# Optimization experiments

Measured on AMD Instinct MI355X. Metric: run time of the kernel, lower is better.

The kernel has to match this reference:

```python
import jax, jax.numpy as jnp
import numpy as np

B = 8          # batch
HID = 1024     # hidden_size
NH = 8         # query heads
KVH = 1        # kv heads (GQA)
HD = 256       # head_dim
NL = 18        # layers
MLP = 4096     # intermediate size
AH = 50        # action_horizon (suffix len)
AD = 32        # action_dim
P = 1037       # prefix_len
EPS = 1e-6
ROPE_BASE = 10000.0
SCALE = HD ** -0.5
NEG = -2.3819763e38


def _rms(x):
    return x * jax.lax.rsqrt(jnp.mean(x * x, axis=-1, keepdims=True) + EPS)


def _ada_norm(x, cond, W):
    # AdaRMS: cond -> (scale, shift, gate); normed*(1+scale)+shift, gate returned for gated residual
    scale, shift, gate = jnp.split(cond @ W, 3, axis=-1)
    return _rms(x) * (1.0 + scale[:, None, :]) + shift[:, None, :], gate[:, None, :]


def _rope(x, pos):
    # x: [B, heads, S, HD], pos: [B, S]; HF rotate-half convention
    inv = 1.0 / (ROPE_BASE ** (jnp.arange(0, HD, 2, dtype=jnp.float32) / HD))
    freqs = pos[:, :, None].astype(jnp.float32) * inv          # [B,S,HD/2]
    cos = jnp.tile(jnp.cos(freqs), (1, 1, 2))[:, None]          # [B,1,S,HD]
    sin = jnp.tile(jnp.sin(freqs), (1, 1, 2))[:, None]
    x1, x2 = jnp.split(x, 2, axis=-1)
    return x * cos + jnp.concatenate([-x2, x1], axis=-1) * sin


def setup_inputs() -> dict:
    key = jax.random.key(0)
    ks = jax.random.split(key, 24)
    s = 0.02
    return {
        'prefix_keys': jax.random.normal(ks[0], (B, NL, KVH, P, HD), jnp.float32),
        'prefix_values': jax.random.normal(ks[1], (B, NL, KVH, P, HD), jnp.float32),
        'prefix_pad_masks': jnp.ones((B, P), dtype=bool),
        'x_t': jax.random.normal(ks[2], (B, AH, AD), jnp.float32),
        'timestep': jax.random.uniform(ks[3], (B,), jnp.float32),
        'Wq': jax.random.normal(ks[4], (NL, HID, NH * HD), jnp.float32) * s,
        'Wk': jax.random.normal(ks[5], (NL, HID, KVH * HD), jnp.float32) * s,
        'Wv': jax.random.normal(ks[6], (NL, HID, KVH * HD), jnp.float32) * s,
        'Wo': jax.random.normal(ks[7], (NL, NH * HD, HID), jnp.float32) * s,
        'Wg': jax.random.normal(ks[8], (NL, HID, MLP), jnp.float32) * s,
        'Wu': jax.random.normal(ks[9], (NL, HID, MLP), jnp.float32) * s,
        'Wd': jax.random.normal(ks[10], (NL, MLP, HID), jnp.float32) * s,
        'A1': jax.random.normal(ks[11], (NL, HID, 3 * HID), jnp.float32) * s,
        'A2': jax.random.normal(ks[12], (NL, HID, 3 * HID), jnp.float32) * s,
        'Af': jax.random.normal(ks[13], (HID, 3 * HID), jnp.float32) * s,
        'W_act_in': jax.random.normal(ks[14], (AD, HID), jnp.float32) * s,
        'b_act_in': jnp.zeros((HID,), jnp.float32),
        'W_act_out': jax.random.normal(ks[15], (HID, AD), jnp.float32) * s,
        'b_act_out': jnp.zeros((AD,), jnp.float32),
        'W_t_in': jax.random.normal(ks[16], (HID, HID), jnp.float32) * s,
        'b_t_in': jnp.zeros((HID,), jnp.float32),
        'W_t_out': jax.random.normal(ks[17], (HID, HID), jnp.float32) * s,
        'b_t_out': jnp.zeros((HID,), jnp.float32),
    }


def reference(prefix_keys, prefix_values, prefix_pad_masks, x_t, timestep,
              Wq, Wk, Wv, Wo, Wg, Wu, Wd, A1, A2, Af,
              W_act_in, b_act_in, W_act_out, b_act_out,
              W_t_in, b_t_in, W_t_out, b_t_out):
    b = x_t.shape[0]
    # --- time embedding (sinusoidal over log-spaced periods) -> AdaRMS cond ---
    frac = jnp.linspace(0.0, 1.0, HID // 2)
    period = 0.004 * (4.0 / 0.004) ** frac
    sin_in = (2.0 * jnp.pi / period)[None, :] * timestep[:, None]
    temb = jnp.concatenate([jnp.sin(sin_in), jnp.cos(sin_in)], axis=1)  # [B,HID]
    cond = jax.nn.silu(jax.nn.silu(temb @ W_t_in + b_t_in) @ W_t_out + b_t_out)

    # --- action input projection ---
    h = x_t @ W_act_in + b_act_in  # [B,AH,HID]

    # --- attention mask & positions ---
    # suffix att_masks = [1,0,...,0] -> cumsum constant -> suffix block fully visible
    suf_att = jnp.ones((b, AH, AH), dtype=bool)
    s2p = jnp.broadcast_to(prefix_pad_masks[:, None, :], (b, AH, P))
    full = jnp.concatenate([s2p, suf_att], axis=2)          # [B,AH,P+AH]
    bias = jnp.where(full, 0.0, NEG).astype(jnp.float32)[:, None]  # [B,1,AH,P+AH]
    offs = jnp.sum(prefix_pad_masks.astype(jnp.int32), axis=-1, keepdims=True)
    pos = offs + jnp.arange(AH)                              # [B,AH]

    def layer(hcur, p):
        wq, wk, wv, wo, wg, wu, wd, a1, a2, ck, cv = p
        normed, gate = _ada_norm(hcur, cond, a1)
        q = (normed @ wq).reshape(b, AH, NH, HD).transpose(0, 2, 1, 3)
        k = (normed @ wk).reshape(b, AH, KVH, HD).transpose(0, 2, 1, 3)
        v = (normed @ wv).reshape(b, AH, KVH, HD).transpose(0, 2, 1, 3)
        q = _rope(q, pos)
        k = _rope(k, pos)
        fk = jnp.concatenate([ck, k], axis=2)   # [B,KVH,P+AH,HD]
        fv = jnp.concatenate([cv, v], axis=2)
        rep = NH // KVH
        fk = jnp.repeat(fk, rep, axis=1)
        fv = jnp.repeat(fv, rep, axis=1)
        scores = jnp.einsum('bhqd,bhkd->bhqk', q, fk) * SCALE + bias
        attn = jax.nn.softmax(scores, axis=-1)
        o = jnp.einsum('bhqk,bhkd->bhqd', attn, fv)
        o = o.transpose(0, 2, 1, 3).reshape(b, AH, NH * HD) @ wo
        h1 = hcur + gate * o                     # gated residual 1
        n2, gate2 = _ada_norm(h1, cond, a2)
        mlp = (jax.nn.gelu(n2 @ wg, approximate=True) * (n2 @ wu)) @ wd
        return h1 + gate2 * mlp, None            # gated residual 2

    pk = jnp.moveaxis(prefix_keys, 1, 0)   # [NL,B,KVH,P,HD]
    pv = jnp.moveaxis(prefix_values, 1, 0)
    h, _ = jax.lax.scan(layer, h, (Wq, Wk, Wv, Wo, Wg, Wu, Wd, A1, A2, pk, pv))

    out, _ = _ada_norm(h, cond, Af)
    return out @ W_act_out + b_act_out  # [B,AH,AD]
```

## Files before the change

### kernel.cpp

```cpp
#include <hip/hip_runtime.h>

typedef unsigned short u16;
typedef unsigned int   u32;
typedef __attribute__((ext_vector_type(8))) short bh8;
typedef __attribute__((ext_vector_type(4))) float f4;

constexpr int BATCH = 8, HIDN = 1024, NHEAD = 8, HD = 256, NLAY = 18, DMLP = 4096;
constexpr int AHOR = 50, ADIMN = 32, PFXN = 1037, SEQN = 1087, NSTR = 17, MR = 400, MP = 512;
constexpr float EPSV = 1e-6f, NEGV = -2.3819763e38f, QSCALE = 0.0625f;
constexpr size_t ADASL = (size_t)37 * 3 * BATCH * HIDN;
constexpr int SW64 = 90, SW32 = 138, SKT = 266, SPT = 74, SVT = 90;

static __device__ __forceinline__ u16 f2bf(float x){
  union{float f; u32 u;} v; v.f = x;
  u32 r = (v.u + 0x7FFFu + ((v.u >> 16) & 1u)) >> 16;
  return (u16)r;
}
static __device__ __forceinline__ float bf2f(u16 u){
  union{u32 u; float f;} v; v.u = ((u32)u) << 16; return v.f;
}
static __device__ __forceinline__ u32 pack2(float a, float b){
  return (u32)f2bf(a) | ((u32)f2bf(b) << 16);
}
static __device__ __forceinline__ f4 MFMA(bh8 a, bh8 b, f4 c){
  return __builtin_amdgcn_mfma_f32_16x16x32_bf16(a, b, c, 0, 0, 0);
}
static __device__ __forceinline__ float siluf_(float x){ return x / (1.f + __expf(-x)); }
static __device__ __forceinline__ float geluf_(float x){
  float y = 0.7978845608028654f * (x + 0.044715f * x * x * x);
  float e = __expf(2.f * y);
  return 0.5f * x * (2.f - 2.f / (e + 1.f));
}

__global__ void k_prep(const int* __restrict__ mask, const float* __restrict__ ts,
                       float* __restrict__ temb, int* __restrict__ offs,
                       float* __restrict__ ropec, float* __restrict__ ropes)
{
  int t = threadIdx.x;
  {
    int b = t >> 5, l = t & 31;
    const int* mp = mask + b * PFXN;
    int s = 0;
    for (int k = l; k < PFXN; k += 32) s += (mp[k] != 0);
    #pragma unroll
    for (int off = 16; off >= 1; off >>= 1) s += __shfl_xor(s, off);
    if (l == 0) offs[b] = s;
  }
  for (int i = t; i < BATCH * 512; i += 256){
    int b = i >> 9, j = i & 511;
    float frac = (float)j * (1.0f / 511.0f);
    float period = 0.004f * __expf(frac * 6.907755278982137f);
    float arg = (6.283185307179586f / period) * ts[b];
    float s, c; sincosf(arg, &s, &c);
    temb[b * HIDN + j] = s;
    temb[b * HIDN + 512 + j] = c;
  }
  __syncthreads();
  for (int i = t; i < BATCH * AHOR * 128; i += 256){
    int d = i & 127, bt = i >> 7, b = bt / AHOR, tt = bt % AHOR;
    float inv = __expf(-((float)d * (1.f / 128.f)) * 9.210340371976184f);
    float arg = (float)(offs[b] + tt) * inv;
// ... 97 lines not shown
  float* hp = h + (size_t)r * HIDN + c0;
  hp[0] = a0; hp[1] = a1; hp[2] = a2; hp[3] = a3;
}

__global__ void k_resnorm(int mode, int np,
    const float* __restrict__ base, const u16* __restrict__ parts,
    const float* __restrict__ gate, const float* __restrict__ sc,
    const float* __restrict__ sh, float* __restrict__ outres,
    u16* __restrict__ fragA)
{
  __shared__ float redl[4];
  int t = threadIdx.x;
  int c = t * 4;
  for (int i = 0; i < 2; ++i){
    int r = blockIdx.x * 2 + i;
    bool live = (r < MR);
    float4 v = {0.f,0.f,0.f,0.f};
    int b = live ? (r / AHOR) : 0;
    if (live){
      v = *(const float4*)(base + (size_t)r * HIDN + c);
      if (mode){
        float s0 = 0, s1 = 0, s2 = 0, s3 = 0;
        #pragma unroll 4
        for (int p = 0; p < np; ++p){
          ushort4 u4 = *(const ushort4*)(parts + ((size_t)p * MP + r) * HIDN + c);
          s0 += bf2f(u4.x); s1 += bf2f(u4.y); s2 += bf2f(u4.z); s3 += bf2f(u4.w);
        }
        float4 gp = *(const float4*)(gate + b * HIDN + c);
        v.x += gp.x * s0; v.y += gp.y * s1; v.z += gp.z * s2; v.w += gp.w * s3;
        *(float4*)(outres + (size_t)r * HIDN + c) = v;
      }
    }
    float ss = v.x*v.x + v.y*v.y + v.z*v.z + v.w*v.w;
    #pragma unroll
    for (int off = 1; off < 64; off <<= 1) ss += __shfl_xor(ss, off);
    if ((t & 63) == 0) redl[t >> 6] = ss;
    __syncthreads();
    float tot = redl[0] + redl[1] + redl[2] + redl[3];
    __syncthreads();
    u16* dst = fragA + ((size_t)(c >> 3)) * MP * 8 + (size_t)r * 8 + (c & 7);
    ushort4 ov;
    if (live){
      float rstd = rsqrtf(tot * (1.0f / HIDN) + EPSV);
      const float4 scp = *(const float4*)(sc + b * HIDN + c);
      const float4 shp = *(const float4*)(sh + b * HIDN + c);
      ov.x = f2bf(v.x * rstd * (1.f + scp.x) + shp.x);
      ov.y = f2bf(v.y * rstd * (1.f + scp.y) + shp.y);
      ov.z = f2bf(v.z * rstd * (1.f + scp.z) + shp.z);
      ov.w = f2bf(v.w * rstd * (1.f + scp.w) + shp.w);
    } else {
      ov.x = ov.y = ov.z = ov.w = 0;
    }
    *(ushort4*)dst = ov;
  }
}

template<int NOUTER>
static __device__ __forceinline__ void gemm_core64(
    const u16* __restrict__ fa,
    const float* __restrict__ Wa, int cb0,
    const float* __restrict__ Wb, int cb1,
    int wN, int kc0, u16* lds, f4 acc[4][4])
{
  const int tid = threadIdx.x;
  const int lane = tid & 63, wave = tid >> 6;
  const int l15 = lane & 15, g = lane >> 4;
  const int wrow = wave * 64;
  const int c4 = (tid & 15) * 4;
  const int r0 = (tid >> 4) * 2;
  const float* wcol = (c4 < 32) ? (Wa + cb0 + c4) : (Wb + cb1 + (c4 - 32));
  const size_t krow0 = (size_t)kc0 * 8 + r0;
  f4 preA[3], preB[3];
  bh8 ab[2][2][4];
  preA[0] = *(const f4*)(wcol + krow0 * wN);
  preB[0] = *(const f4*)(wcol + (krow0 + 1) * wN);
  #pragma unroll
  for (int kk = 0; kk < 2; ++kk){
    const u16* ap = fa + ((size_t)(kc0 + kk * 4 + g) * MP + wrow + l15) * 8;
    #pragma unroll
    for (int mf = 0; mf < 4; ++mf) ab[0][kk][mf] = *(const bh8*)(ap + mf * 128);
  }
  if (NOUTER > 1){
    preA[1] = *(const f4*)(wcol + (krow0 + 64) * wN);
    preB[1] = *(const f4*)(wcol + (krow0 + 65) * wN);
  }
  if (NOUTER > 2){
    preA[2] = *(const f4*)(wcol + (krow0 + 128) * wN);
    preB[2] = *(const f4*)(wcol + (krow0 + 129) * wN);
  }
  #pragma unroll
  for (int i = 0; i < 4; ++i)
    *(u32*)(lds + (c4 + i) * SW64 + r0) = pack2(preA[0][i], preB[0][i]);
  __syncthreads();
  #pragma unroll
  for (int ko = 0; ko < NOUTER; ++ko){
    u16* ldsr = lds + (ko & 1) * (64 * SW64);
    if (ko + 1 < NOUTER){
      #pragma unroll
      for (int kk = 0; kk < 2; ++kk){
        const u16* ap = fa + ((size_t)(kc0 + (ko + 1) * 8 + kk * 4 + g) * MP + wrow + l15) * 8;
        #pragma unroll
        for (int mf = 0; mf < 4; ++mf) ab[(ko + 1) & 1][kk][mf] = *(const bh8*)(ap + mf * 128);
      }
    }
    if (ko + 3 < NOUTER){
      preA[ko % 3] = *(const f4*)(wcol + (krow0 + (size_t)(ko + 3) * 64) * wN);
      preB[ko % 3] = *(const f4*)(wcol + (krow0 + (size_t)(ko + 3) * 64 + 1) * wN);
    }
    #pragma unroll
    for (int kk = 0; kk < 2; ++kk){
      bh8 bb[4];
      #pragma unroll
      for (int nf = 0; nf < 4; ++nf) bb[nf] = *(const bh8*)(ldsr + (nf * 16 + l15) * SW64 + kk * 32 + g * 8);
      #pragma unroll
      for (int mf = 0; mf < 4; ++mf)
        #pragma unroll
        for (int nf = 0; nf < 4; ++nf)
          acc[mf][nf] = MFMA(ab[ko & 1][kk][mf], bb[nf], acc[mf][nf]);
    }
    if (ko + 1 < NOUTER){
      u16* ldsw = lds + ((ko + 1) & 1) * (64 * SW64);
      const int sl = (ko + 1) % 3;
      #pragma unroll
      for (int i = 0; i < 4; ++i)
        *(u32*)(ldsw + (c4 + i) * SW64 + r0) = pack2(preA[sl][i], preB[sl][i]);
      __syncthreads();
    }
  }
}

template<int NOUTER>
static __device__ __forceinline__ void gemm_core32w(
    const u16* __restrict__ fa,
    const float* __restrict__ Wa, int cb0,
    const float* __restrict__ Wb, int cb1,
    int wN, u16* lds, f4 acc[4][2])
{
  const int tid = threadIdx.x;
  const int lane = tid & 63, wave = tid >> 6;
  const int l15 = lane & 15, g = lane >> 4;
  const int wrow = wave * 64;
  const int c4 = (tid & 7) * 4;
  const int r0 = (tid >> 3) * 2;
  const float* wcol = (c4 < 16) ? (Wa + cb0 + c4) : (Wb + cb1 + (c4 - 16));
  f4 preA[3], preB[3];
  preA[0] = *(const f4*)(wcol + (size_t)r0 * wN);
  preB[0] = *(const f4*)(wcol + (size_t)(r0 + 1) * wN);
  if (NOUTER > 1){
    preA[1] = *(const f4*)(wcol + (size_t)(128 + r0) * wN);
    preB[1] = *(const f4*)(wcol + (size_t)(129 + r0) * wN);
  }
  if (NOUTER > 2){
    preA[2] = *(const f4*)(wcol + (size_t)(256 + r0) * wN);
    preB[2] = *(const f4*)(wcol + (size_t)(257 + r0) * wN);
  }
  #pragma unroll
  for (int i = 0; i < 4; ++i)
    *(u32*)(lds + (c4 + i) * SW32 + r0) = pack2(preA[0][i], preB[0][i]);
  __syncthreads();
  #pragma unroll
  for (int ko = 0; ko < NOUTER; ++ko){
    u16* ldsr = lds + (ko & 1) * (32 * SW32);
    bh8 a01[2][4], a23[2][4];
    #pragma unroll
    for (int kk = 0; kk < 2; ++kk){
      const u16* ap = fa + ((size_t)(ko * 16 + kk * 4 + g) * MP + wrow + l15) * 8;
      #pragma unroll
      for (int mf = 0; mf < 4; ++mf) a01[kk][mf] = *(const bh8*)(ap + mf * 128);
    }
    if (ko + 3 < NOUTER){
      preA[ko % 3] = *(const f4*)(wcol + (size_t)((ko + 3) * 128 + r0) * wN);
      preB[ko % 3] = *(const f4*)(wcol + (size_t)((ko + 3) * 128 + r0 + 1) * wN);
    }
    #pragma unroll
    for (int kk = 2; kk < 4; ++kk){
      const u16* ap = fa + ((size_t)(ko * 16 + kk * 4 + g) * MP + wrow + l15) * 8;
      #pragma unroll
      for (int mf = 0; mf < 4; ++mf) a23[kk - 2][mf] = *(const bh8*)(ap + mf * 128);
    }
    #pragma unroll
// ... 44 lines not shown
  f4 acc[4][2];
  #pragma unroll
  for (int i = 0; i < 4; ++i)
    #pragma unroll
    for (int j = 0; j < 2; ++j) acc[i][j] = (f4){0.f, 0.f, 0.f, 0.f};
  gemm_core32w<8>(n1, Wa, cb0, Wb, cb1, wN, lds, acc);
  int tid = threadIdx.x, lane = tid & 63, wave = tid >> 6, l15 = lane & 15, g = lane >> 4;
  int wrow = wave * 64;
  #pragma unroll
  for (int mf = 0; mf < 4; ++mf)
    #pragma unroll
    for (int r = 0; r < 4; ++r){
      int row = wrow + mf * 16 + 4 * g + r;
      if (row >= MR) continue;
      int b = row / AHOR, tt = row - b * AHOR;
      float lo = acc[mf][0][r], hi = acc[mf][1][r];
      if (type == 2){
        size_t vb = ((size_t)(b * AHOR + tt)) * HD;
        vs[vb + d0 + l15] = f2bf(lo);
        vs[vb + d0 + 16 + l15] = f2bf(hi);
      } else {
        int dA = fb + l15;
        float cz = ropec[(size_t)(b * AHOR + tt) * 128 + dA];
        float sz = ropes[(size_t)(b * AHOR + tt) * 128 + dA];
        float oA = lo * cz - hi * sz;
        float oB = hi * cz + lo * sz;
        if (type == 0){
          oA *= QSCALE; oB *= QSCALE;
          int rowp = head * AHOR + tt;
          int dB = dA + 128;
          qf[((size_t)(b * 32 + (dA >> 3))) * MP * 8 + (size_t)rowp * 8 + (dA & 7)] = f2bf(oA);
          qf[((size_t)(b * 32 + (dB >> 3))) * MP * 8 + (size_t)rowp * 8 + (dB & 7)] = f2bf(oB);
        } else {
          size_t kb = ((size_t)(b * AHOR + tt)) * HD;
          ks[kb + dA] = f2bf(oA);
          ks[kb + dA + 128] = f2bf(oB);
        }
      }
    }
}

__global__ __launch_bounds__(512) void k_attn(
    const u16* __restrict__ qf, const u16* __restrict__ kss, const u16* __restrict__ vss,
    const float* __restrict__ pk, const float* __restrict__ pv,
    const int* __restrict__ mask, int layer,
    u16* __restrict__ opart, float* __restrict__ mrow, float* __restrict__ lrow)
{
  __shared__ u16 kv[256 * SVT];
  __shared__ u16 plds[256 * SPT];
  int s = blockIdx.x, b = blockIdx.y, z = blockIdx.z;
  int tid = threadIdx.x, lane = tid & 63, wave = tid >> 6, l15 = lane & 15, g = lane >> 4;
  int zb = z * 256;
  int wbase = wave * 32;
  {
    int key = tid >> 3, dblk = (tid & 7) * 32;
    int kg = s * 64 + key;
    u32* dst = (u32*)(kv + key * SKT + dblk);
    if (kg < PFXN){
      const float4* src = (const float4*)(pk + (((size_t)b * NLAY + layer) * PFXN + kg) * HD + dblk);
      #pragma unroll
      for (int j = 0; j < 8; ++j){ float4 v = src[j]; dst[2*j] = pack2(v.x, v.y); dst[2*j+1] = pack2(v.z, v.w); }
    } else if (kg < SEQN){
      const u32* src = (const u32*)(kss + ((size_t)b * AHOR + (kg - PFXN)) * HD + dblk);
      #pragma unroll
      for (int j = 0; j < 16; ++j) dst[j] = src[j];
    } else {
      #pragma unroll
      for (int j = 0; j < 16; ++j) dst[j] = 0;
    }
  }
  float vreg[32];
  int vkey = tid >> 3, vdb = (tid & 7) * 32;
  {
    int kgv = s * 64 + vkey;
    if (kgv < PFXN){
      const float4* src = (const float4*)(pv + (((size_t)b * NLAY + layer) * PFXN + kgv) * HD + vdb);
      #pragma unroll
      for (int j = 0; j < 8; ++j){ float4 v = src[j]; vreg[4*j] = v.x; vreg[4*j+1] = v.y; vreg[4*j+2] = v.z; vreg[4*j+3] = v.w; }
    } else if (kgv < SEQN){
      const u32* src = (const u32*)(vss + ((size_t)b * AHOR + (kgv - PFXN)) * HD + vdb);
      #pragma unroll
      for (int j = 0; j < 16; ++j){ u32 u = src[j]; vreg[2*j] = bf2f((u16)(u & 0xFFFF)); vreg[2*j+1] = bf2f((u16)(u >> 16)); }
    } else {
      #pragma unroll
      for (int j = 0; j < 32; ++j) vreg[j] = 0.f;
    }
  }
  bool valid[4];
  #pragma unroll
  for (int nf = 0; nf < 4; ++nf){
    int kgc = s * 64 + nf * 16 + l15;
    valid[nf] = (kgc < PFXN) ? (mask[b * PFXN + kgc] != 0) : (kgc < SEQN);
  }
  __syncthreads();
  f4 acc[2][4];
  #pragma unroll
  for (int i = 0; i < 2; ++i)
    #pragma unroll
    for (int j = 0; j < 4; ++j) acc[i][j] = (f4){0.f,0.f,0.f,0.f};
  const u16* qb = qf + (size_t)b * 32 * MP * 8;
  #pragma unroll
  for (int ko = 0; ko < 4; ++ko)
    #pragma unroll
    for (int kk = 0; kk < 2; ++kk){
      int kc = ko * 8 + kk * 4 + g;
      bh8 a[2], bb[4];
      const u16* ap = qb + ((size_t)kc * MP + zb + wbase + l15) * 8;
      #pragma unroll
      for (int mf = 0; mf < 2; ++mf) a[mf] = *(const bh8*)(ap + mf * 128);
      #pragma unroll
      for (int nf = 0; nf < 4; ++nf) bb[nf] = *(const bh8*)(kv + (nf * 16 + l15) * SKT + ko * 64 + kk * 32 + g * 8);
      #pragma unroll
      for (int mf = 0; mf < 2; ++mf)
        #pragma unroll
        for (int nf = 0; nf < 4; ++nf) acc[mf][nf] = MFMA(a[mf], bb[nf], acc[mf][nf]);
    }
  #pragma unroll
  for (int nf = 0; nf < 4; ++nf) if (!valid[nf]){
    #pragma unroll
    for (int mf = 0; mf < 2; ++mf){
      acc[mf][nf][0] = NEGV; acc[mf][nf][1] = NEGV; acc[mf][nf][2] = NEGV; acc[mf][nf][3] = NEGV;
    }
  }
  #pragma unroll
  for (int mf = 0; mf < 2; ++mf)
    #pragma unroll
    for (int r = 0; r < 4; ++r){
      float m0 = fmaxf(fmaxf(acc[mf][0][r], acc[mf][1][r]), fmaxf(acc[mf][2][r], acc[mf][3][r]));
      #pragma unroll
      for (int off = 1; off < 16; off <<= 1) m0 = fmaxf(m0, __shfl_xor(m0, off));
      int lr = wbase + mf * 16 + 4 * g + r;
      float sum = 0.f;
      #pragma unroll
      for (int nf = 0; nf < 4; ++nf){
        float p = __expf(acc[mf][nf][r] - m0);
        sum += p;
        plds[lr * SPT + nf * 16 + l15] = f2bf(p);
      }
      #pragma unroll
      for (int off = 1; off < 16; off <<= 1) sum += __shfl_xor(sum, off);
      if (l15 == 0){
        mrow[((size_t)b * NSTR + s) * MP + zb + lr] = m0;
        lrow[((size_t)b * NSTR + s) * MP + zb + lr] = sum;
      }
    }
  __syncthreads();
  {
    #pragma unroll
    for (int j = 0; j < 32; ++j){
      int dloc = vdb + j;
      kv[dloc * SVT + ((dloc >> 5) & 3) * 8 + vkey] = f2bf(vreg[j]);
    }
  }
  __syncthreads();
  #pragma unroll
  for (int dc = 0; dc < 4; ++dc){
    f4 oc[2][4];
    #pragma unroll
    for (int i = 0; i < 2; ++i)
      #pragma unroll
      for (int j = 0; j < 4; ++j) oc[i][j] = (f4){0.f,0.f,0.f,0.f};
    #pragma unroll
    for (int kk = 0; kk < 2; ++kk){
      bh8 a[2], bb[4];
      #pragma unroll
      for (int mf = 0; mf < 2; ++mf) a[mf] = *(const bh8*)(plds + (wbase + mf * 16 + l15) * SPT + kk * 32 + g * 8);
      #pragma unroll
      for (int nf = 0; nf < 4; ++nf){
        int dcol = dc * 64 + nf * 16 + l15;
        bb[nf] = *(const bh8*)(kv + dcol * SVT + ((dcol >> 5) & 3) * 8 + kk * 32 + g * 8);
      }
      #pragma unroll
      for (int mf = 0; mf < 2; ++mf)
        #pragma unroll
        for (int nf = 0; nf < 4; ++nf) oc[mf][nf] = MFMA(a[mf], bb[nf], oc[mf][nf]);
    }
    #pragma unroll
    for (int mf = 0; mf < 2; ++mf)
      #pragma unroll
      for (int r = 0; r < 4; ++r){
        int row = zb + wbase + mf * 16 + 4 * g + r;
        if (row < MR){
          #pragma unroll
          for (int nf = 0; nf < 4; ++nf){
            int d = dc * 64 + nf * 16 + l15;
            opart[(((size_t)b * NSTR + s) * MR + row) * HD + d] = f2bf(oc[mf][nf][r]);
          }
        }
      }
  }
}

__global__ void k_comb(const u16* __restrict__ opart, const float* __restrict__ mrow,
                       const float* __restrict__ lrow, u16* __restrict__ ao)
{
  int b = blockIdx.y;
  int t = threadIdx.x;
  int d4 = (t & 63) * 4;
  int row = blockIdx.x * 4 + (t >> 6);
  float M = -3.0e38f;
  for (int s2 = 0; s2 < NSTR; ++s2) M = fmaxf(M, mrow[((size_t)b * NSTR + s2) * MP + row]);
  float L = 0.f;
  float o0 = 0.f, o1 = 0.f, o2 = 0.f, o3 = 0.f;
  for (int s2 = 0; s2 < NSTR; ++s2){
    float w = __expf(mrow[((size_t)b * NSTR + s2) * MP + row] - M);
    L += w * lrow[((size_t)b * NSTR + s2) * MP + row];
    ushort4 u4 = *(const ushort4*)(opart + (((size_t)b * NSTR + s2) * MR + row) * HD + d4);
    o0 += w * bf2f(u4.x); o1 += w * bf2f(u4.y); o2 += w * bf2f(u4.z); o3 += w * bf2f(u4.w);
  }
  float rL = 1.0f / L;
  int h = row / AHOR, tt = row - h * AHOR;
  int col = h * HD + d4;
  int rg = b * AHOR + tt;
  ushort4 ov;
  ov.x = f2bf(o0 * rL); ov.y = f2bf(o1 * rL); ov.z = f2bf(o2 * rL); ov.w = f2bf(o3 * rL);
  *(ushort4*)(ao + ((size_t)(col >> 3)) * MP * 8 + (size_t)rg * 8 + (col & 7)) = ov;
}

template<int NOUTER>
__global__ __launch_bounds__(512) void k_gemm_part(
    const u16* __restrict__ fa, const float* __restrict__ W, int wN,
    int kcPerSlice, u16* __restrict__ outp)
{
  __shared__ u16 lds[2 * 64 * SW64];
  int n0 = blockIdx.x * 64;
  int ksl = blockIdx.y;
  f4 acc[4][4];
  #pragma unroll
  for (int i = 0; i < 4; ++i)
    #pragma unroll
    for (int j = 0; j < 4; ++j) acc[i][j] = (f4){0.f,0.f,0.f,0.f};
  gemm_core64<NOUTER>(fa, W, n0, W, n0 + 32, wN, ksl * kcPerSlice, lds, acc);
  int tid = threadIdx.x, lane = tid & 63, wave = tid >> 6, l15 = lane & 15, g = lane >> 4;
  int wrow = wave * 64;
  #pragma unroll
  for (int mf = 0; mf < 4; ++mf)
    #pragma unroll
    for (int r = 0; r < 4; ++r){
      int row = wrow + mf * 16 + 4 * g + r;
      #pragma unroll
      for (int nf = 0; nf < 4; ++nf)
        outp[((size_t)ksl * MP + row) * 1024 + n0 + nf * 16 + l15] = f2bf(acc[mf][nf][r]);
    }
}

__global__ __launch_bounds__(512) void k_mlpup(
    const u16* __restrict__ n2, const float* __restrict__ Wg, const float* __restrict__ Wu,
    u16* __restrict__ mlpf)
{
  __shared__ u16 lds[2 * 32 * SW32];
  int n0 = blockIdx.x * 16;
  f4 acc[4][2];
  #pragma unroll
  for (int i = 0; i < 4; ++i)
    #pragma unroll
    for (int j = 0; j < 2; ++j) acc[i][j] = (f4){0.f,0.f,0.f,0.f};
  gemm_core32w<8>(n2, Wg, n0, Wu, n0, DMLP, lds, acc);
  int tid = threadIdx.x, lane = tid & 63, wave = tid >> 6, l15 = lane & 15, g = lane >> 4;
  int wrow = wave * 64;
  #pragma unroll
  for (int mf = 0; mf < 4; ++mf)
    #pragma unroll
    for (int r = 0; r < 4; ++r){
      int row = wrow + mf * 16 + 4 * g + r;
      int col = n0 + l15;
      float gg = acc[mf][0][r], uu = acc[mf][1][r];
      float act = geluf_(gg) * uu;
      mlpf[((size_t)(col >> 3)) * MP * 8 + (size_t)row * 8 + (col & 7)] = f2bf(act);
    }
}

__global__ void k_out(const u16* __restrict__ nfr, const float* __restrict__ W,
                      const float* __restrict__ bias, float* __restrict__ out)
{
  int t = threadIdx.x;
  int row = blockIdx.x * 8 + (t >> 5);
  int c = t & 31;
  float acc = bias[c];
  for (int kc = 0; kc < 128; ++kc){
    bh8 v = *(const bh8*)(nfr + ((size_t)kc * MP + row) * 8);
    #pragma unroll
    for (int j = 0; j < 8; ++j)
      acc += bf2f((u16)v[j]) * W[(kc * 8 + j) * ADIMN + c];
  }
  out[row * ADIMN + c] = acc;
}

extern "C" void kernel_launch(void* const* d_in, const int* in_sizes, int n_in,
                              void* d_out, int out_size, void* d_ws, size_t ws_size,
                              hipStream_t stream)
{
  const float* pk  = (const float*)d_in[0];
  const float* pv  = (const float*)d_in[1];
  const int*   msk = (const int*)d_in[2];
  const float* xt  = (const float*)d_in[3];
  const float* ts  = (const float*)d_in[4];
  const float* Wq  = (const float*)d_in[5];
  const float* Wk  = (const float*)d_in[6];
  const float* Wv  = (const float*)d_in[7];
  const float* Wo  = (const float*)d_in[8];
  const float* Wg  = (const float*)d_in[9];
  const float* Wu  = (const float*)d_in[10];
  const float* Wd  = (const float*)d_in[11];
  const float* A1  = (const float*)d_in[12];
  const float* A2  = (const float*)d_in[13];
  const float* Af  = (const float*)d_in[14];
  const float* Wai = (const float*)d_in[15];
  const float* bai = (const float*)d_in[16];
  const float* Wao = (const float*)d_in[17];
  const float* bao = (const float*)d_in[18];
  const float* Wti = (const float*)d_in[19];
  const float* bti = (const float*)d_in[20];
  const float* Wto = (const float*)d_in[21];
  const float* bto = (const float*)d_in[22];

  char* w = (char*)d_ws;
  size_t off = 0;
  auto alloc = [&](size_t bytes) -> char* {
    char* p = w + off; off += (bytes + 255) & ~(size_t)255; return p;
  };
  float* temb  = (float*)alloc((size_t)BATCH * HIDN * 4);
  float* ttmp  = (float*)alloc((size_t)BATCH * HIDN * 4);
  float* cond  = (float*)alloc((size_t)BATCH * HIDN * 4);
  int*   offs  = (int*)alloc(BATCH * 4);
  float* ropec = (float*)alloc((size_t)BATCH * AHOR * 128 * 4);
  float* ropes = (float*)alloc((size_t)BATCH * AHOR * 128 * 4);
  float* ada   = (float*)alloc(ADASL * 4);
  float* adap  = (float*)alloc(8 * ADASL * 4);
  float* h     = (float*)alloc((size_t)MR * HIDN * 4);
  float* h1    = (float*)alloc((size_t)MR * HIDN * 4);
  u16*   n1    = (u16*)alloc((size_t)128 * MP * 8 * 2);
  u16*   n2    = (u16*)alloc((size_t)128 * MP * 8 * 2);
  u16*   qf    = (u16*)alloc((size_t)BATCH * 32 * MP * 8 * 2);
  u16*   kss   = (u16*)alloc((size_t)BATCH * AHOR * HD * 2);
  u16*   vss   = (u16*)alloc((size_t)BATCH * AHOR * HD * 2);
  u16*   opart = (u16*)alloc((size_t)BATCH * NSTR * MR * HD * 2);
  float* mrow  = (float*)alloc((size_t)BATCH * NSTR * MP * 4);
  float* lrow  = (float*)alloc((size_t)BATCH * NSTR * MP * 4);
  u16*   ao    = (u16*)alloc((size_t)256 * MP * 8 * 2);
  u16*   opp   = (u16*)alloc((size_t)16 * MP * 1024 * 2);
  u16*   mlpf  = (u16*)alloc((size_t)512 * MP * 8 * 2);
  u16*   mdp   = (u16*)alloc((size_t)16 * MP * 1024 * 2);
  if (off > ws_size) return;

  k_prep<<<1, 256, 0, stream>>>(msk, ts, temb, offs, ropec, ropes);
  k_tproj<<<32, 256, 0, stream>>>(temb, Wti, bti, ttmp);
  k_tproj<<<32, 256, 0, stream>>>(ttmp, Wto, bto, cond);
  k_ada_part<<<dim3(3, 37, 8), 256, 0, stream>>>(cond, A1, A2, Af, adap);
  k_ada_red<<<444, 256, 0, stream>>>(adap, ada);
  k_hin<<<MR, 256, 0, stream>>>(xt, Wai, bai, h);

  auto AP = [&](int y, int comp){ return ada + ((size_t)y * 3 + comp) * BATCH * HIDN; };

  k_resnorm<<<256, 256, 0, stream>>>(0, 0, h, nullptr, nullptr, AP(0,0), AP(0,1), nullptr, n1);

  for (int l = 0; l < NLAY; ++l){
    k_qkvrope<<<80, 512, 0, stream>>>(n1, Wq + (size_t)l * HIDN * NHEAD * HD,
                                      Wk + (size_t)l * HIDN * HD, Wv + (size_t)l * HIDN * HD,
                                      ropec, ropes, qf, kss, vss);
    k_attn<<<dim3(NSTR, BATCH, 2), 512, 0, stream>>>(qf, kss, vss, pk, pv, msk, l, opart, mrow, lrow);
    k_comb<<<dim3(100, BATCH), 256, 0, stream>>>(opart, mrow, lrow, ao);
    k_gemm_part<2><<<dim3(16, 16), 512, 0, stream>>>(ao, Wo + (size_t)l * 2048 * 1024, 1024, 16, opp);
    k_resnorm<<<256, 256, 0, stream>>>(1, 16, h, opp, AP(l,2), AP(NLAY+l,0), AP(NLAY+l,1), h1, n2);
    k_mlpup<<<256, 512, 0, stream>>>(n2, Wg + (size_t)l * HIDN * DMLP, Wu + (size_t)l * HIDN * DMLP, mlpf);
    k_gemm_part<4><<<dim3(16, 16), 512, 0, stream>>>(mlpf, Wd + (size_t)l * DMLP * 1024, 1024, 32, mdp);
    const float* nsc = (l < NLAY - 1) ? AP(l + 1, 0) : AP(36, 0);
    const float* nsh = (l < NLAY - 1) ? AP(l + 1, 1) : AP(36, 1);
    k_resnorm<<<256, 256, 0, stream>>>(2, 16, h1, mdp, AP(NLAY+l,2), nsc, nsh, h, n1);
  }
  k_out<<<50, 256, 0, stream>>>(n1, Wao, bao, (float*)d_out);
}
```

Baseline: 2.912 ms.

## Process two key tiles per attention block with online softmax, halve split-K partials

The attention kernel now walks two 64-key tiles per block, keeping a running max and sum and rescaling the output accumulators (online softmax). The grid drops from 17 to 9 key groups, so fewer partial outputs are written and combined. Separately, the Wo and Wd split-K GEMMs use 8 slices instead of 16, each doing twice the K work, which halves the partial buffers the residual-norm kernels must read. The cost is fewer blocks in flight on a large GPU and more registers per attention thread for the four-chunk output accumulators.

```diff
diff --git a/kernel.cpp b/kernel.cpp
--- a/kernel.cpp
+++ b/kernel.cpp
@@ -6,7 +6,8 @@
 typedef __attribute__((ext_vector_type(4))) float f4;
 
 constexpr int BATCH = 8, HIDN = 1024, NHEAD = 8, HD = 256, NLAY = 18, DMLP = 4096;
-constexpr int AHOR = 50, ADIMN = 32, PFXN = 1037, SEQN = 1087, NSTR = 17, MR = 400, MP = 512;
+constexpr int AHOR = 50, ADIMN = 32, PFXN = 1037, SEQN = 1087, MR = 400, MP = 512;
+constexpr int NGRP = 9;
 constexpr float EPSV = 1e-6f, NEGV = -2.3819763e38f, QSCALE = 0.0625f;
 constexpr size_t ADASL = (size_t)37 * 3 * BATCH * HIDN;
 constexpr int SW64 = 90, SW32 = 138, SKT = 266, SPT = 74, SVT = 90;
@@ -434,129 +435,159 @@
   int tid = threadIdx.x, lane = tid & 63, wave = tid >> 6, l15 = lane & 15, g = lane >> 4;
   int zb = z * 256;
   int wbase = wave * 32;
-  {
-    int key = tid >> 3, dblk = (tid & 7) * 32;
-    int kg = s * 64 + key;
-    u32* dst = (u32*)(kv + key * SKT + dblk);
-    if (kg < PFXN){
-      const float4* src = (const float4*)(pk + (((size_t)b * NLAY + layer) * PFXN + kg) * HD + dblk);
-      #pragma unroll
-      for (int j = 0; j < 8; ++j){ float4 v = src[j]; dst[2*j] = pack2(v.x, v.y); dst[2*j+1] = pack2(v.z, v.w); }
-    } else if (kg < SEQN){
-      const u32* src = (const u32*)(kss + ((size_t)b * AHOR + (kg - PFXN)) * HD + dblk);
-      #pragma unroll
-      for (int j = 0; j < 16; ++j) dst[j] = src[j];
-    } else {
-      #pragma unroll
-      for (int j = 0; j < 16; ++j) dst[j] = 0;
-    }
-  }
-  float vreg[32];
-  int vkey = tid >> 3, vdb = (tid & 7) * 32;
-  {
-    int kgv = s * 64 + vkey;
-    if (kgv < PFXN){
-      const float4* src = (const float4*)(pv + (((size_t)b * NLAY + layer) * PFXN + kgv) * HD + vdb);
-      #pragma unroll
-      for (int j = 0; j < 8; ++j){ float4 v = src[j]; vreg[4*j] = v.x; vreg[4*j+1] = v.y; vreg[4*j+2] = v.z; vreg[4*j+3] = v.w; }
-    } else if (kgv < SEQN){
-      const u32* src = (const u32*)(vss + ((size_t)b * AHOR + (kgv - PFXN)) * HD + vdb);
-      #pragma unroll
-      for (int j = 0; j < 16; ++j){ u32 u = src[j]; vreg[2*j] = bf2f((u16)(u & 0xFFFF)); vreg[2*j+1] = bf2f((u16)(u >> 16)); }
-    } else {
-      #pragma unroll
-      for (int j = 0; j < 32; ++j) vreg[j] = 0.f;
-    }
-  }
-  bool valid[4];
-  #pragma unroll
-  for (int nf = 0; nf < 4; ++nf){
-    int kgc = s * 64 + nf * 16 + l15;
-    valid[nf] = (kgc < PFXN) ? (mask[b * PFXN + kgc] != 0) : (kgc < SEQN);
-  }
-  __syncthreads();
-  f4 acc[2][4];
-  #pragma unroll
-  for (int i = 0; i < 2; ++i)
-    #pragma unroll
-    for (int j = 0; j < 4; ++j) acc[i][j] = (f4){0.f,0.f,0.f,0.f};
-  const u16* qb = qf + (size_t)b * 32 * MP * 8;
-  #pragma unroll
-  for (int ko = 0; ko < 4; ++ko)
-    #pragma unroll
-    for (int kk = 0; kk < 2; ++kk){
-      int kc = ko * 8 + kk * 4 + g;
-      bh8 a[2], bb[4];
-      const u16* ap = qb + ((size_t)kc * MP + zb + wbase + l15) * 8;
-      #pragma unroll
-      for (int mf = 0; mf < 2; ++mf) a[mf] = *(const bh8*)(ap + mf * 128);
-      #pragma unroll
-      for (int nf = 0; nf < 4; ++nf) bb[nf] = *(const bh8*)(kv + (nf * 16 + l15) * SKT + ko * 64 + kk * 32 + g * 8);
-      #pragma unroll
-      for (int mf = 0; mf < 2; ++mf)
-        #pragma unroll
-        for (int nf = 0; nf < 4; ++nf) acc[mf][nf] = MFMA(a[mf], bb[nf], acc[mf][nf]);
-    }
-  #pragma unroll
-  for (int nf = 0; nf < 4; ++nf) if (!valid[nf]){
-    #pragma unroll
-    for (int mf = 0; mf < 2; ++mf){
-      acc[mf][nf][0] = NEGV; acc[mf][nf][1] = NEGV; acc[mf][nf][2] = NEGV; acc[mf][nf][3] = NEGV;
-    }
-  }
+  f4 oc[4][2][4];
+  #pragma unroll
+  for (int dc = 0; dc < 4; ++dc)
+    #pragma unroll
+    for (int mf = 0; mf < 2; ++mf)
+      #pragma unroll
+      for (int nf = 0; nf < 4; ++nf) oc[dc][mf][nf] = (f4){0.f,0.f,0.f,0.f};
+  float mrun[2][4], lrun[2][4];
   #pragma unroll
   for (int mf = 0; mf < 2; ++mf)
     #pragma unroll
+    for (int r = 0; r < 4; ++r){ mrun[mf][r] = -3.0e38f; lrun[mf][r] = 0.f; }
+
+  #pragma unroll
+  for (int kt = 0; kt < 2; ++kt){
+    int kbase = s * 128 + kt * 64;
+    {
+      int key = tid >> 3, dblk = (tid & 7) * 32;
+      int kg = kbase + key;
+      u32* dst = (u32*)(kv + key * SKT + dblk);
+      if (kg < PFXN){
+        const float4* src = (const float4*)(pk + (((size_t)b * NLAY + layer) * PFXN + kg) * HD + dblk);
+        #pragma unroll
+        for (int j = 0; j < 8; ++j){ float4 v = src[j]; dst[2*j] = pack2(v.x, v.y); dst[2*j+1] = pack2(v.z, v.w); }
+      } else if (kg < SEQN){
+        const u32* src = (const u32*)(kss + ((size_t)b * AHOR + (kg - PFXN)) * HD + dblk);
+        #pragma unroll
+        for (int j = 0; j < 16; ++j) dst[j] = src[j];
+      } else {
+        #pragma unroll
+        for (int j = 0; j < 16; ++j) dst[j] = 0;
+      }
+    }
+    float vreg[32];
+    int vkey = tid >> 3, vdb = (tid & 7) * 32;
+    {
+      int kgv = kbase + vkey;
+      if (kgv < PFXN){
+        const float4* src = (const float4*)(pv + (((size_t)b * NLAY + layer) * PFXN + kgv) * HD + vdb);
+        #pragma unroll
+        for (int j = 0; j < 8; ++j){ float4 v = src[j]; vreg[4*j] = v.x; vreg[4*j+1] = v.y; vreg[4*j+2] = v.z; vreg[4*j+3] = v.w; }
+      } else if (kgv < SEQN){
+        const u32* src = (const u32*)(vss + ((size_t)b * AHOR + (kgv - PFXN)) * HD + vdb);
+        #pragma unroll
+        for (int j = 0; j < 16; ++j){ u32 u = src[j]; vreg[2*j] = bf2f((u16)(u & 0xFFFF)); vreg[2*j+1] = bf2f((u16)(u >> 16)); }
+      } else {
+        #pragma unroll
+        for (int j = 0; j < 32; ++j) vreg[j] = 0.f;
+      }
+    }
+    bool valid[4];
+    #pragma unroll
+    for (int nf = 0; nf < 4; ++nf){
+      int kgc = kbase + nf * 16 + l15;
+      valid[nf] = (kgc < PFXN) ? (mask[b * PFXN + kgc] != 0) : (kgc < SEQN);
+    }
+    __syncthreads();
+    f4 acc[2][4];
+    #pragma unroll
+    for (int i = 0; i < 2; ++i)
+      #pragma unroll
+      for (int j = 0; j < 4; ++j) acc[i][j] = (f4){0.f,0.f,0.f,0.f};
+    const u16* qb = qf + (size_t)b * 32 * MP * 8;
+    #pragma unroll
+    for (int ko = 0; ko < 4; ++ko)
+      #pragma unroll
+      for (int kk = 0; kk < 2; ++kk){
+        int kc = ko * 8 + kk * 4 + g;
+        bh8 a[2], bb[4];
+        const u16* ap = qb + ((size_t)kc * MP + zb + wbase + l15) * 8;
+        #pragma unroll
+        for (int mf = 0; mf < 2; ++mf) a[mf] = *(const bh8*)(ap + mf * 128);
+        #pragma unroll
+        for (int nf = 0; nf < 4; ++nf) bb[nf] = *(const bh8*)(kv + (nf * 16 + l15) * SKT + ko * 64 + kk * 32 + g * 8);
+        #pragma unroll
+        for (int mf = 0; mf < 2; ++mf)
+          #pragma unroll
+          for (int nf = 0; nf < 4; ++nf) acc[mf][nf] = MFMA(a[mf], bb[nf], acc[mf][nf]);
+      }
+    #pragma unroll
+    for (int nf = 0; nf < 4; ++nf) if (!valid[nf]){
+      #pragma unroll
+      for (int mf = 0; mf < 2; ++mf){
+        acc[mf][nf][0] = NEGV; acc[mf][nf][1] = NEGV; acc[mf][nf][2] = NEGV; acc[mf][nf][3] = NEGV;
+      }
+    }
+    #pragma unroll
+    for (int mf = 0; mf < 2; ++mf)
+      #pragma unroll
+      for (int r = 0; r < 4; ++r){
+        float mt = fmaxf(fmaxf(acc[mf][0][r], acc[mf][1][r]), fmaxf(acc[mf][2][r], acc[mf][3][r]));
+        #pragma unroll
+        for (int off = 1; off < 16; off <<= 1) mt = fmaxf(mt, __shfl_xor(mt, off));
+        float mnew = fmaxf(mrun[mf][r], mt);
+        float alpha = __expf(mrun[mf][r] - mnew);
+        int lr = wbase + mf * 16 + 4 * g + r;
+        float sum = 0.f;
+        #pragma unroll
+        for (int nf = 0; nf < 4; ++nf){
+          float p = __expf(acc[mf][nf][r] - mnew);
+          sum += p;
+          plds[lr * SPT + nf * 16 + l15] = f2bf(p);
+        }
+        #pragma unroll
+        for (int off = 1; off < 16; off <<= 1) sum += __shfl_xor(sum, off);
+        lrun[mf][r] = alpha * lrun[mf][r] + sum;
+        mrun[mf][r] = mnew;
+        #pragma unroll
+        for (int dc = 0; dc < 4; ++dc)
+          #pragma unroll
+          for (int nf = 0; nf < 4; ++nf) oc[dc][mf][nf][r] *= alpha;
+      }
+    __syncthreads();
+    {
+      #pragma unroll
+      for (int j = 0; j < 32; ++j){
+        int dloc = vdb + j;
+        kv[dloc * SVT + ((dloc >> 5) & 3) * 8 + vkey] = f2bf(vreg[j]);
+      }
+    }
+    __syncthreads();
+    #pragma unroll
+    for (int dc = 0; dc < 4; ++dc){
+      #pragma unroll
+      for (int kk = 0; kk < 2; ++kk){
+        bh8 a[2], bb[4];
+        #pragma unroll
+        for (int mf = 0; mf < 2; ++mf) a[mf] = *(const bh8*)(plds + (wbase + mf * 16 + l15) * SPT + kk * 32 + g * 8);
+        #pragma unroll
+        for (int nf = 0; nf < 4; ++nf){
+          int dcol = dc * 64 + nf * 16 + l15;
+          bb[nf] = *(const bh8*)(kv + dcol * SVT + ((dcol >> 5) & 3) * 8 + kk * 32 + g * 8);
+        }
+        #pragma unroll
+        for (int mf = 0; mf < 2; ++mf)
+          #pragma unroll
+          for (int nf = 0; nf < 4; ++nf) oc[dc][mf][nf] = MFMA(a[mf], bb[nf], oc[dc][mf][nf]);
+      }
+    }
+    __syncthreads();
+  }
+  #pragma unroll
+  for (int mf = 0; mf < 2; ++mf)
+    #pragma unroll
     for (int r = 0; r < 4; ++r){
-      float m0 = fmaxf(fmaxf(acc[mf][0][r], acc[mf][1][r]), fmaxf(acc[mf][2][r], acc[mf][3][r]));
-      #pragma unroll
-      for (int off = 1; off < 16; off <<= 1) m0 = fmaxf(m0, __shfl_xor(m0, off));
       int lr = wbase + mf * 16 + 4 * g + r;
-      float sum = 0.f;
-      #pragma unroll
-      for (int nf = 0; nf < 4; ++nf){
-        float p = __expf(acc[mf][nf][r] - m0);
-        sum += p;
-        plds[lr * SPT + nf * 16 + l15] = f2bf(p);
-      }
-      #pragma unroll
-      for (int off = 1; off < 16; off <<= 1) sum += __shfl_xor(sum, off);
       if (l15 == 0){
-        mrow[((size_t)b * NSTR + s) * MP + zb + lr] = m0;
-        lrow[((size_t)b * NSTR + s) * MP + zb + lr] = sum;
-      }
-    }
-  __syncthreads();
-  {
-    #pragma unroll
-    for (int j = 0; j < 32; ++j){
-      int dloc = vdb + j;
-      kv[dloc * SVT + ((dloc >> 5) & 3) * 8 + vkey] = f2bf(vreg[j]);
-    }
-  }
-  __syncthreads();
-  #pragma unroll
-  for (int dc = 0; dc < 4; ++dc){
-    f4 oc[2][4];
-    #pragma unroll
-    for (int i = 0; i < 2; ++i)
-      #pragma unroll
-      for (int j = 0; j < 4; ++j) oc[i][j] = (f4){0.f,0.f,0.f,0.f};
-    #pragma unroll
-    for (int kk = 0; kk < 2; ++kk){
-      bh8 a[2], bb[4];
-      #pragma unroll
-      for (int mf = 0; mf < 2; ++mf) a[mf] = *(const bh8*)(plds + (wbase + mf * 16 + l15) * SPT + kk * 32 + g * 8);
-      #pragma unroll
-      for (int nf = 0; nf < 4; ++nf){
-        int dcol = dc * 64 + nf * 16 + l15;
-        bb[nf] = *(const bh8*)(kv + dcol * SVT + ((dcol >> 5) & 3) * 8 + kk * 32 + g * 8);
-      }
-      #pragma unroll
-      for (int mf = 0; mf < 2; ++mf)
-        #pragma unroll
-        for (int nf = 0; nf < 4; ++nf) oc[mf][nf] = MFMA(a[mf], bb[nf], oc[mf][nf]);
-    }
+        mrow[((size_t)b * NGRP + s) * MP + zb + lr] = mrun[mf][r];
+        lrow[((size_t)b * NGRP + s) * MP + zb + lr] = lrun[mf][r];
+      }
+    }
+  #pragma unroll
+  for (int dc = 0; dc < 4; ++dc)
     #pragma unroll
     for (int mf = 0; mf < 2; ++mf)
       #pragma unroll
@@ -566,11 +597,10 @@
           #pragma unroll
           for (int nf = 0; nf < 4; ++nf){
             int d = dc * 64 + nf * 16 + l15;
-            opart[(((size_t)b * NSTR + s) * MR + row) * HD + d] = f2bf(oc[mf][nf][r]);
+            opart[(((size_t)b * NGRP + s) * MR + row) * HD + d] = f2bf(oc[dc][mf][nf][r]);
           }
         }
       }
-  }
 }
 
 __global__ void k_comb(const u16* __restrict__ opart, const float* __restrict__ mrow,
@@ -581,13 +611,13 @@
   int d4 = (t & 63) * 4;
   int row = blockIdx.x * 4 + (t >> 6);
   float M = -3.0e38f;
-  for (int s2 = 0; s2 < NSTR; ++s2) M = fmaxf(M, mrow[((size_t)b * NSTR + s2) * MP + row]);
+  for (int s2 = 0; s2 < NGRP; ++s2) M = fmaxf(M, mrow[((size_t)b * NGRP + s2) * MP + row]);
   float L = 0.f;
   float o0 = 0.f, o1 = 0.f, o2 = 0.f, o3 = 0.f;
-  for (int s2 = 0; s2 < NSTR; ++s2){
-    float w = __expf(mrow[((size_t)b * NSTR + s2) * MP + row] - M);
-    L += w * lrow[((size_t)b * NSTR + s2) * MP + row];
-    ushort4 u4 = *(const ushort4*)(opart + (((size_t)b * NSTR + s2) * MR + row) * HD + d4);
+  for (int s2 = 0; s2 < NGRP; ++s2){
+    float w = __expf(mrow[((size_t)b * NGRP + s2) * MP + row] - M);
+    L += w * lrow[((size_t)b * NGRP + s2) * MP + row];
+    ushort4 u4 = *(const ushort4*)(opart + (((size_t)b * NGRP + s2) * MR + row) * HD + d4);
     o0 += w * bf2f(u4.x); o1 += w * bf2f(u4.y); o2 += w * bf2f(u4.z); o3 += w * bf2f(u4.w);
   }
   float rL = 1.0f / L;
@@ -716,13 +746,13 @@
   u16*   qf    = (u16*)alloc((size_t)BATCH * 32 * MP * 8 * 2);
   u16*   kss   = (u16*)alloc((size_t)BATCH * AHOR * HD * 2);
   u16*   vss   = (u16*)alloc((size_t)BATCH * AHOR * HD * 2);
-  u16*   opart = (u16*)alloc((size_t)BATCH * NSTR * MR * HD * 2);
-  float* mrow  = (float*)alloc((size_t)BATCH * NSTR * MP * 4);
-  float* lrow  = (float*)alloc((size_t)BATCH * NSTR * MP * 4);
+  u16*   opart = (u16*)alloc((size_t)BATCH * NGRP * MR * HD * 2);
+  float* mrow  = (float*)alloc((size_t)BATCH * NGRP * MP * 4);
+  float* lrow  = (float*)alloc((size_t)BATCH * NGRP * MP * 4);
   u16*   ao    = (u16*)alloc((size_t)256 * MP * 8 * 2);
-  u16*   opp   = (u16*)alloc((size_t)16 * MP * 1024 * 2);
+  u16*   opp   = (u16*)alloc((size_t)8 * MP * 1024 * 2);
   u16*   mlpf  = (u16*)alloc((size_t)512 * MP * 8 * 2);
-  u16*   mdp   = (u16*)alloc((size_t)16 * MP * 1024 * 2);
+  u16*   mdp   = (u16*)alloc((size_t)8 * MP * 1024 * 2);
   if (off > ws_size) return;
 
   k_prep<<<1, 256, 0, stream>>>(msk, ts, temb, offs, ropec, ropes);
@@ -740,15 +770,15 @@
     k_qkvrope<<<80, 512, 0, stream>>>(n1, Wq + (size_t)l * HIDN * NHEAD * HD,
                                       Wk + (size_t)l * HIDN * HD, Wv + (size_t)l * HIDN * HD,
                                       ropec, ropes, qf, kss, vss);
-    k_attn<<<dim3(NSTR, BATCH, 2), 512, 0, stream>>>(qf, kss, vss, pk, pv, msk, l, opart, mrow, lrow);
+    k_attn<<<dim3(NGRP, BATCH, 2), 512, 0, stream>>>(qf, kss, vss, pk, pv, msk, l, opart, mrow, lrow);
     k_comb<<<dim3(100, BATCH), 256, 0, stream>>>(opart, mrow, lrow, ao);
-    k_gemm_part<2><<<dim3(16, 16), 512, 0, stream>>>(ao, Wo + (size_t)l * 2048 * 1024, 1024, 16, opp);
-    k_resnorm<<<256, 256, 0, stream>>>(1, 16, h, opp, AP(l,2), AP(NLAY+l,0), AP(NLAY+l,1), h1, n2);
+    k_gemm_part<4><<<dim3(16, 8), 512, 0, stream>>>(ao, Wo + (size_t)l * 2048 * 1024, 1024, 32, opp);
+    k_resnorm<<<256, 256, 0, stream>>>(1, 8, h, opp, AP(l,2), AP(NLAY+l,0), AP(NLAY+l,1), h1, n2);
     k_mlpup<<<256, 512, 0, stream>>>(n2, Wg + (size_t)l * HIDN * DMLP, Wu + (size_t)l * HIDN * DMLP, mlpf);
-    k_gemm_part<4><<<dim3(16, 16), 512, 0, stream>>>(mlpf, Wd + (size_t)l * DMLP * 1024, 1024, 32, mdp);
+    k_gemm_part<8><<<dim3(16, 8), 512, 0, stream>>>(mlpf, Wd + (size_t)l * DMLP * 1024, 1024, 64, mdp);
     const float* nsc = (l < NLAY - 1) ? AP(l + 1, 0) : AP(36, 0);
     const float* nsh = (l < NLAY - 1) ? AP(l + 1, 1) : AP(36, 1);
-    k_resnorm<<<256, 256, 0, stream>>>(2, 16, h1, mdp, AP(NLAY+l,2), nsc, nsh, h, n1);
+    k_resnorm<<<256, 256, 0, stream>>>(2, 8, h1, mdp, AP(NLAY+l,2), nsc, nsh, h, n1);
   }
   k_out<<<50, 256, 0, stream>>>(n1, Wao, bao, (float*)d_out);
 }
```

Measured after the change: 2.991 ms. +2.7%, slower.

## Use 32-wide N tiles with 8 K-slices for Wo and Wd GEMMs

Applied to the files above, without the earlier changes.

Replaces the 64-column split-K GEMM core with the existing 32-wide core for the attention output and MLP down projections. The grid becomes 32 column tiles by 8 K-slices instead of 16 by 16, so each block covers twice the K depth and the partial-sum buffers and resnorm reduction shrink from 16 to 8 slices. This cuts the bf16 partial traffic and reduction work. Block count stays the same, but each block now owns half as many output columns, which may reduce MFMA reuse per LDS tile.

```diff
diff --git a/kernel.cpp b/kernel.cpp
--- a/kernel.cpp
+++ b/kernel.cpp
@@ -210,80 +210,6 @@
       ov.x = ov.y = ov.z = ov.w = 0;
     }
     *(ushort4*)dst = ov;
-  }
-}
-
-template<int NOUTER>
-static __device__ __forceinline__ void gemm_core64(
-    const u16* __restrict__ fa,
-    const float* __restrict__ Wa, int cb0,
-    const float* __restrict__ Wb, int cb1,
-    int wN, int kc0, u16* lds, f4 acc[4][4])
-{
-  const int tid = threadIdx.x;
-  const int lane = tid & 63, wave = tid >> 6;
-  const int l15 = lane & 15, g = lane >> 4;
-  const int wrow = wave * 64;
-  const int c4 = (tid & 15) * 4;
-  const int r0 = (tid >> 4) * 2;
-  const float* wcol = (c4 < 32) ? (Wa + cb0 + c4) : (Wb + cb1 + (c4 - 32));
-  const size_t krow0 = (size_t)kc0 * 8 + r0;
-  f4 preA[3], preB[3];
-  bh8 ab[2][2][4];
-  preA[0] = *(const f4*)(wcol + krow0 * wN);
-  preB[0] = *(const f4*)(wcol + (krow0 + 1) * wN);
-  #pragma unroll
-  for (int kk = 0; kk < 2; ++kk){
-    const u16* ap = fa + ((size_t)(kc0 + kk * 4 + g) * MP + wrow + l15) * 8;
-    #pragma unroll
-    for (int mf = 0; mf < 4; ++mf) ab[0][kk][mf] = *(const bh8*)(ap + mf * 128);
-  }
-  if (NOUTER > 1){
-    preA[1] = *(const f4*)(wcol + (krow0 + 64) * wN);
-    preB[1] = *(const f4*)(wcol + (krow0 + 65) * wN);
-  }
-  if (NOUTER > 2){
-    preA[2] = *(const f4*)(wcol + (krow0 + 128) * wN);
-    preB[2] = *(const f4*)(wcol + (krow0 + 129) * wN);
-  }
-  #pragma unroll
-  for (int i = 0; i < 4; ++i)
-    *(u32*)(lds + (c4 + i) * SW64 + r0) = pack2(preA[0][i], preB[0][i]);
-  __syncthreads();
-  #pragma unroll
-  for (int ko = 0; ko < NOUTER; ++ko){
-    u16* ldsr = lds + (ko & 1) * (64 * SW64);
-    if (ko + 1 < NOUTER){
-      #pragma unroll
-      for (int kk = 0; kk < 2; ++kk){
-        const u16* ap = fa + ((size_t)(kc0 + (ko + 1) * 8 + kk * 4 + g) * MP + wrow + l15) * 8;
-        #pragma unroll
-        for (int mf = 0; mf < 4; ++mf) ab[(ko + 1) & 1][kk][mf] = *(const bh8*)(ap + mf * 128);
-      }
-    }
-    if (ko + 3 < NOUTER){
-      preA[ko % 3] = *(const f4*)(wcol + (krow0 + (size_t)(ko + 3) * 64) * wN);
-      preB[ko % 3] = *(const f4*)(wcol + (krow0 + (size_t)(ko + 3) * 64 + 1) * wN);
-    }
-    #pragma unroll
-    for (int kk = 0; kk < 2; ++kk){
-      bh8 bb[4];
-      #pragma unroll
-      for (int nf = 0; nf < 4; ++nf) bb[nf] = *(const bh8*)(ldsr + (nf * 16 + l15) * SW64 + kk * 32 + g * 8);
-      #pragma unroll
-      for (int mf = 0; mf < 4; ++mf)
-        #pragma unroll
-        for (int nf = 0; nf < 4; ++nf)
-          acc[mf][nf] = MFMA(ab[ko & 1][kk][mf], bb[nf], acc[mf][nf]);
-    }
-    if (ko + 1 < NOUTER){
-      u16* ldsw = lds + ((ko + 1) & 1) * (64 * SW64);
-      const int sl = (ko + 1) % 3;
-      #pragma unroll
-      for (int i = 0; i < 4; ++i)
-        *(u32*)(ldsw + (c4 + i) * SW64 + r0) = pack2(preA[sl][i], preB[sl][i]);
-      __syncthreads();
-    }
   }
 }
 
@@ -600,19 +526,21 @@
 }
 
 template<int NOUTER>
-__global__ __launch_bounds__(512) void k_gemm_part(
+__global__ __launch_bounds__(512) void k_gemm_part32(
     const u16* __restrict__ fa, const float* __restrict__ W, int wN,
-    int kcPerSlice, u16* __restrict__ outp)
-{
-  __shared__ u16 lds[2 * 64 * SW64];
-  int n0 = blockIdx.x * 64;
+    u16* __restrict__ outp)
+{
+  __shared__ u16 lds[2 * 32 * SW32];
+  int n0 = blockIdx.x * 32;
   int ksl = blockIdx.y;
-  f4 acc[4][4];
+  const u16* fa_s = fa + (size_t)(ksl * NOUTER * 16) * MP * 8;
+  const float* W_s = W + (size_t)(ksl * NOUTER * 128) * wN;
+  f4 acc[4][2];
   #pragma unroll
   for (int i = 0; i < 4; ++i)
     #pragma unroll
-    for (int j = 0; j < 4; ++j) acc[i][j] = (f4){0.f,0.f,0.f,0.f};
-  gemm_core64<NOUTER>(fa, W, n0, W, n0 + 32, wN, ksl * kcPerSlice, lds, acc);
+    for (int j = 0; j < 2; ++j) acc[i][j] = (f4){0.f,0.f,0.f,0.f};
+  gemm_core32w<NOUTER>(fa_s, W_s, n0, W_s, n0 + 16, wN, lds, acc);
   int tid = threadIdx.x, lane = tid & 63, wave = tid >> 6, l15 = lane & 15, g = lane >> 4;
   int wrow = wave * 64;
   #pragma unroll
@@ -620,9 +548,8 @@
     #pragma unroll
     for (int r = 0; r < 4; ++r){
       int row = wrow + mf * 16 + 4 * g + r;
-      #pragma unroll
-      for (int nf = 0; nf < 4; ++nf)
-        outp[((size_t)ksl * MP + row) * 1024 + n0 + nf * 16 + l15] = f2bf(acc[mf][nf][r]);
+      outp[((size_t)ksl * MP + row) * 1024 + n0 + l15] = f2bf(acc[mf][0][r]);
+      outp[((size_t)ksl * MP + row) * 1024 + n0 + 16 + l15] = f2bf(acc[mf][1][r]);
     }
 }
 
@@ -720,9 +647,9 @@
   float* mrow  = (float*)alloc((size_t)BATCH * NSTR * MP * 4);
   float* lrow  = (float*)alloc((size_t)BATCH * NSTR * MP * 4);
   u16*   ao    = (u16*)alloc((size_t)256 * MP * 8 * 2);
-  u16*   opp   = (u16*)alloc((size_t)16 * MP * 1024 * 2);
+  u16*   opp   = (u16*)alloc((size_t)8 * MP * 1024 * 2);
   u16*   mlpf  = (u16*)alloc((size_t)512 * MP * 8 * 2);
-  u16*   mdp   = (u16*)alloc((size_t)16 * MP * 1024 * 2);
+  u16*   mdp   = (u16*)alloc((size_t)8 * MP * 1024 * 2);
   if (off > ws_size) return;
 
   k_prep<<<1, 256, 0, stream>>>(msk, ts, temb, offs, ropec, ropes);
@@ -742,13 +669,13 @@
                                       ropec, ropes, qf, kss, vss);
     k_attn<<<dim3(NSTR, BATCH, 2), 512, 0, stream>>>(qf, kss, vss, pk, pv, msk, l, opart, mrow, lrow);
     k_comb<<<dim3(100, BATCH), 256, 0, stream>>>(opart, mrow, lrow, ao);
-    k_gemm_part<2><<<dim3(16, 16), 512, 0, stream>>>(ao, Wo + (size_t)l * 2048 * 1024, 1024, 16, opp);
-    k_resnorm<<<256, 256, 0, stream>>>(1, 16, h, opp, AP(l,2), AP(NLAY+l,0), AP(NLAY+l,1), h1, n2);
+    k_gemm_part32<2><<<dim3(32, 8), 512, 0, stream>>>(ao, Wo + (size_t)l * 2048 * 1024, 1024, opp);
+    k_resnorm<<<256, 256, 0, stream>>>(1, 8, h, opp, AP(l,2), AP(NLAY+l,0), AP(NLAY+l,1), h1, n2);
     k_mlpup<<<256, 512, 0, stream>>>(n2, Wg + (size_t)l * HIDN * DMLP, Wu + (size_t)l * HIDN * DMLP, mlpf);
-    k_gemm_part<4><<<dim3(16, 16), 512, 0, stream>>>(mlpf, Wd + (size_t)l * DMLP * 1024, 1024, 32, mdp);
+    k_gemm_part32<4><<<dim3(32, 8), 512, 0, stream>>>(mlpf, Wd + (size_t)l * DMLP * 1024, 1024, mdp);
     const float* nsc = (l < NLAY - 1) ? AP(l + 1, 0) : AP(36, 0);
     const float* nsh = (l < NLAY - 1) ? AP(l + 1, 1) : AP(36, 1);
-    k_resnorm<<<256, 256, 0, stream>>>(2, 16, h1, mdp, AP(NLAY+l,2), nsc, nsh, h, n1);
+    k_resnorm<<<256, 256, 0, stream>>>(2, 8, h1, mdp, AP(NLAY+l,2), nsc, nsh, h, n1);
   }
   k_out<<<50, 256, 0, stream>>>(n1, Wao, bao, (float*)d_out);
 }
```

Result: faster. 2.832 ms (-2.8%).
